# Kernel optimization log

Hardware: AMD Instinct MI355X
Metric: run time of the kernel (lower is better)

The kernel has to match this reference:

```python
import math
import jax, jax.numpy as jnp
import numpy as np

NUM_HEADS = 8
HEAD_DIM = 64
SCALE = 1.0 / math.sqrt(HEAD_DIM)


def setup_inputs() -> dict:
    key = jax.random.key(0)
    k1, k2, k3, k4 = jax.random.split(key, 4)
    B, C, H, W = 8, 256, 32, 32
    hidden = NUM_HEADS * HEAD_DIM  # 512
    x = jax.random.normal(k1, (B, C, H, W), dtype=jnp.float32)
    Wqkv = jax.random.normal(k2, (3 * hidden, C), dtype=jnp.float32) * 0.02  # 1x1 conv, no bias
    Wout = jax.random.normal(k3, (C, hidden), dtype=jnp.float32) * 0.02      # 1x1 conv weight
    bout = jax.random.normal(k4, (C,), dtype=jnp.float32) * 0.02             # 1x1 conv bias
    return {"x": x, "Wqkv": Wqkv, "Wout": Wout, "bout": bout}


def reference(x, Wqkv, Wout, bout):
    B, C, H, W = x.shape
    n = H * W
    # _AttLayer: 1x1 conv -> channels ordered (k=3, heads, head_dim)
    qkv = jnp.einsum('bcxy,oc->boxy', x, Wqkv)            # [B, 3*h*d, H, W]
    qkv = qkv.reshape(B, 3, NUM_HEADS, HEAD_DIM, n)       # 'b (k h d) x y -> b k h d (x y)'
    Q, K, V = qkv[:, 0], qkv[:, 1], qkv[:, 2]             # each [B, h, d, n]
    # CalcAtt: scaled QK^T, stable softmax over j, then Att @ V
    att = jnp.einsum('bhdi,bhdj->bhij', Q, K) * SCALE     # [B, h, n, n]
    att = jax.nn.softmax(att, axis=-1)                    # softmax already subtracts amax
    out = jnp.einsum('bhij,bhdj->bhid', att, V)           # [B, h, n, d]
    # 'b h (x y) d -> b (h d) x y'
    out = out.transpose(0, 1, 3, 2).reshape(B, NUM_HEADS * HEAD_DIM, H, W)
    # _AttOutLayer: 1x1 conv with bias
    return jnp.einsum('boxy,co->bcxy', out, Wout) + bout[None, :, None, None]
```

## Files before the change

kernel.cpp:

```cpp
#include <hip/hip_runtime.h>
#include <math.h>

#define NH 8
#define HD 64
#define NTOK 1024
#define CIN 256
#define HIDDEN 512
#define O3 1536
#define BATCH 8
#define ATT_SCALE 0.125f

typedef unsigned short u16;
typedef __attribute__((ext_vector_type(8))) short s16x8;
typedef __attribute__((ext_vector_type(4))) float f32x4;
typedef __attribute__((ext_vector_type(4))) unsigned short u16x4;

__device__ __forceinline__ u16 f2bf(float f) {
    union { float f; unsigned int u; } v; v.f = f;
    v.u += 0x7fff + ((v.u >> 16) & 1);
    return (u16)(v.u >> 16);
}
__device__ __forceinline__ float bf2f(u16 h) {
    union { unsigned int u; float f; } v; v.u = (unsigned)h << 16;
    return v.f;
}
__device__ __forceinline__ void split2(float x, u16& hi, u16& lo) {
    const u16 h = f2bf(x);
    hi = h;
    lo = f2bf(x - bf2f(h));
}

__device__ __forceinline__ s16x8 ldf(const u16* buf, int row, int chunk) {
    const int byte = (row * 128 + chunk * 16) ^ ((row & 7) << 4);
    return *(const s16x8*)((const char*)buf + byte);
}
__device__ __forceinline__ void st32(u16* buf, int row, int ch, s16x8 a, s16x8 b) {
    char* p = (char*)buf;
    *(s16x8*)(p + ((row * 128 + ch * 32) ^ ((row & 7) << 4)))      = a;
    *(s16x8*)(p + ((row * 128 + ch * 32 + 16) ^ ((row & 7) << 4))) = b;
}
__device__ __forceinline__ void st_stage(u16* buf, int t, s16x8 v0, s16x8 v1) {
    const int row = t >> 2, ch = t & 3;
    *(s16x8*)((char*)buf + ((row * 128 + ch * 16)       ^ ((row & 7) << 4))) = v0;
    *(s16x8*)((char*)buf + ((row * 128 + (ch + 4) * 16) ^ ((row & 7) << 4))) = v1;
}
__device__ __forceinline__ float hmax4(f32x4 v) {
    return fmaxf(fmaxf(v[0], v[1]), fmaxf(v[2], v[3]));
}
__device__ __forceinline__ float hsum4(f32x4 v) {
    return (v[0] + v[1]) + (v[2] + v[3]);
}

__global__ __launch_bounds__(256)
void split_f32(const float* __restrict__ src, u16* __restrict__ hi,
               u16* __restrict__ lo, int n4)
{
    const int i = blockIdx.x * 256 + threadIdx.x;
    if (i >= n4) return;
    const float4 v = ((const float4*)src)[i];
    u16 h0,h1,h2,h3,l0,l1,l2,l3;
    split2(v.x,h0,l0); split2(v.y,h1,l1); split2(v.z,h2,l2); split2(v.w,h3,l3);
    u16x4 H = {h0,h1,h2,h3}, L = {l0,l1,l2,l3};
    ((u16x4*)hi)[i] = H;
    ((u16x4*)lo)[i] = L;
}

__global__ __launch_bounds__(256)
void xpose_x(const float* __restrict__ x, u16* __restrict__ xthi,
             u16* __restrict__ xtlo)
{
    __shared__ float T[64][68];
    const int t  = threadIdx.x;
    const int p0 = blockIdx.x * 64;
    const int c0 = blockIdx.y * 64;
    const int b  = blockIdx.z;
    const int cl = t >> 4, pj = (t & 15) * 4;
    #pragma unroll
    for (int k = 0; k < 4; ++k)
        *(float4*)&T[cl + 16 * k][pj] =
            *(const float4*)&x[((size_t)b * CIN + c0 + cl + 16 * k) * NTOK + p0 + pj];
    __syncthreads();
    const int p = t >> 2, ch = t & 3;
    u16* dhi = xthi + ((size_t)b * NTOK + p0 + p) * CIN + c0 + ch * 16;
    u16* dlo = xtlo + ((size_t)b * NTOK + p0 + p) * CIN + c0 + ch * 16;
    #pragma unroll
    for (int g = 0; g < 2; ++g) {
        s16x8 H, L;
        #pragma unroll
        for (int e = 0; e < 8; ++e) {
            u16 hh, ll;
            split2(T[ch * 16 + g * 8 + e][p], hh, ll);
            H[e] = (short)hh; L[e] = (short)ll;
        }
        *(s16x8*)(dhi + g * 8) = H;
        *(s16x8*)(dlo + g * 8) = L;
    }
}

__global__ __launch_bounds__(256, 4)
void gemm_qkv_mfma(const u16* __restrict__ Whi, const u16* __restrict__ Wlo,
                   const u16* __restrict__ Xhi, const u16* __restrict__ Xlo,
                   u16* __restrict__ qkt, u16* __restrict__ vd)
{
    __shared__ __align__(16) char smem[32768];
    u16* Ah = (u16*)smem;
    u16* Al = (u16*)(smem + 8192);
    u16* Bh = (u16*)(smem + 16384);
    u16* Bl = (u16*)(smem + 24576);

    const int t = threadIdx.x;
    const int lane = t & 63, w = t >> 6;
    const int lr = lane & 15, lq = lane >> 4;
    const int p0 = blockIdx.x * 64;
    const int m0 = blockIdx.y * 64;
    const int b  = blockIdx.z;
    const int row = t >> 2, ch = t & 3;

    const u16* wh = Whi + (size_t)(m0 + row) * CIN + ch * 16;
    const u16* wl = Wlo + (size_t)(m0 + row) * CIN + ch * 16;
    const u16* xh = Xhi + ((size_t)b * NTOK + p0 + row) * CIN + ch * 16;
    const u16* xl = Xlo + ((size_t)b * NTOK + p0 + row) * CIN + ch * 16;

    f32x4 acc[4] = {};
    for (int kc = 0; kc < CIN; kc += 64) {
        __syncthreads();
        st32(Ah, row, ch, *(const s16x8*)(wh + kc), *(const s16x8*)(wh + kc + 8));
        st32(Al, row, ch, *(const s16x8*)(wl + kc), *(const s16x8*)(wl + kc + 8));
        st32(Bh, row, ch, *(const s16x8*)(xh + kc), *(const s16x8*)(xh + kc + 8));
        st32(Bl, row, ch, *(const s16x8*)(xl + kc), *(const s16x8*)(xl + kc + 8));
        __syncthreads();
        #pragma unroll
        for (int ks = 0; ks < 2; ++ks) {
            const s16x8 ah = ldf(Ah, w * 16 + lr, ks * 4 + lq);
            const s16x8 al = ldf(Al, w * 16 + lr, ks * 4 + lq);
            #pragma unroll
            for (int js = 0; js < 4; ++js) {
                const s16x8 bh = ldf(Bh, js * 16 + lr, ks * 4 + lq);
                const s16x8 bl = ldf(Bl, js * 16 + lr, ks * 4 + lq);
                acc[js] = __builtin_amdgcn_mfma_f32_16x16x32_bf16(ah, bh, acc[js], 0, 0, 0);
                acc[js] = __builtin_amdgcn_mfma_f32_16x16x32_bf16(al, bh, acc[js], 0, 0, 0);
                acc[js] = __builtin_amdgcn_mfma_f32_16x16x32_bf16(ah, bl, acc[js], 0, 0, 0);
            }
        }
    }

    __syncthreads();
    u16* T = Ah;
    char* Tc = (char*)T;
    if (m0 < 1024) {
        const float scale = (m0 < 512) ? ATT_SCALE : 1.0f;
        #pragma unroll
        for (int js = 0; js < 4; ++js) {
            const int p = js * 16 + lr;
            #pragma unroll
            for (int r = 0; r < 4; ++r) {
                const int o = w * 16 + lq * 4 + r;
                *(u16*)(Tc + ((p * 128 + o * 2) ^ ((p & 7) << 4))) = f2bf(acc[js][r] * scale);
            }
        }
        __syncthreads();
        const int sidx = (m0 < 512) ? 0 : 1;
        const int h = (m0 & 511) >> 6;
        u16* dst = qkt + ((((size_t)b * 2 + sidx) * NH + h) * NTOK + p0 + row) * 64 + ch * 16;
        *(s16x8*)dst       = *(const s16x8*)(Tc + ((row * 128 + ch * 32)      ^ ((row & 7) << 4)));
        *(s16x8*)(dst + 8) = *(const s16x8*)(Tc + ((row * 128 + ch * 32 + 16) ^ ((row & 7) << 4)));
    } else {
        const int h = (m0 - 1024) >> 6;
        #pragma unroll
        for (int js = 0; js < 4; ++js) {
            const int p = js * 16 + lr;
            #pragma unroll
            for (int r = 0; r < 4; ++r) {
                const int o = w * 16 + lq * 4 + r;
                *(u16*)(Tc + ((o * 128 + p * 2) ^ ((o & 7) << 4))) = f2bf(acc[js][r]);
            }
        }
        __syncthreads();
        u16* dst = vd + (((size_t)b * NH + h) * 64 + row) * NTOK + p0 + ch * 16;
        *(s16x8*)dst       = *(const s16x8*)(Tc + ((row * 128 + ch * 32)      ^ ((row & 7) << 4)));
        *(s16x8*)(dst + 8) = *(const s16x8*)(Tc + ((row * 128 + ch * 32 + 16) ^ ((row & 7) << 4)));
    }
}

__global__ __launch_bounds__(256, 4)
void attn_kernel(const u16* __restrict__ qkt, const u16* __restrict__ vd,
                 float* __restrict__ attn_out)
{
    __shared__ __align__(16) u16 Qt[64 * 64];
    __shared__ __align__(16) u16 Kt[64 * 64];
    __shared__ __align__(16) u16 Vt[64 * 64];
    __shared__ __align__(16) u16 Ps[64 * 64];

    const int t    = threadIdx.x;
    const int lane = t & 63;
    const int w    = t >> 6;
    const int lr   = lane & 15;
    const int lq   = lane >> 4;

    const int bid     = blockIdx.x;
    const int logical = (bid & 7) * 128 + (bid >> 3);
    const int it = logical & 15;
    const int h  = (logical >> 4) & 7;
    const int b  = logical >> 7;
    const int i0 = it * 64;

    const int srow = t >> 2, sch = t & 3;
    const u16* qg = qkt + ((((size_t)b * 2 + 0) * NH + h) * NTOK + i0 + srow) * 64 + sch * 8;
    const u16* kg = qkt + ((((size_t)b * 2 + 1) * NH + h) * NTOK + srow) * 64 + sch * 8;
    const u16* vg = vd  + (((size_t)b * NH + h) * 64 + srow) * NTOK + sch * 8;

    st_stage(Qt, t, *(const s16x8*)qg, *(const s16x8*)(qg + 32));

    s16x8 k0 = *(const s16x8*)kg, k1 = *(const s16x8*)(kg + 32);
    s16x8 v0 = *(const s16x8*)vg, v1 = *(const s16x8*)(vg + 32);

    f32x4 o0 = {0.f,0.f,0.f,0.f}, o1 = o0, o2 = o0, o3 = o0;
    float m_run = -INFINITY, l_run = 0.0f;

    const int ii = w * 16 + lr;
    char* pr = (char*)Ps;

    for (int jt = 0; jt < 16; ++jt) {
        __syncthreads();
        st_stage(Kt, t, k0, k1);
        st_stage(Vt, t, v0, v1);
        const int jn = (jt + 1) & 15;
        k0 = *(const s16x8*)(kg + (size_t)jn * 4096);
        k1 = *(const s16x8*)(kg + (size_t)jn * 4096 + 32);
        v0 = *(const s16x8*)(vg + (size_t)jn * 64);
        v1 = *(const s16x8*)(vg + (size_t)jn * 64 + 32);
        __syncthreads();

        f32x4 s0 = {0.f,0.f,0.f,0.f}, s1 = s0, s2 = s0, s3 = s0;
        #pragma unroll
        for (int ks = 0; ks < 2; ++ks) {
            const s16x8 qb = ldf(Qt, w * 16 + lr, ks * 4 + lq);
            s0 = __builtin_amdgcn_mfma_f32_16x16x32_bf16(ldf(Kt,      lr, ks*4+lq), qb, s0, 0,0,0);
            s1 = __builtin_amdgcn_mfma_f32_16x16x32_bf16(ldf(Kt, 16 + lr, ks*4+lq), qb, s1, 0,0,0);
            s2 = __builtin_amdgcn_mfma_f32_16x16x32_bf16(ldf(Kt, 32 + lr, ks*4+lq), qb, s2, 0,0,0);
            s3 = __builtin_amdgcn_mfma_f32_16x16x32_bf16(ldf(Kt, 48 + lr, ks*4+lq), qb, s3, 0,0,0);
        }

        float mt = fmaxf(fmaxf(hmax4(s0), hmax4(s1)), fmaxf(hmax4(s2), hmax4(s3)));
        mt = fmaxf(mt, __shfl_xor(mt, 16));
        mt = fmaxf(mt, __shfl_xor(mt, 32));
        const float mnew = fmaxf(m_run, mt);
        const float corr = __expf(m_run - mnew);
        f32x4 p0v, p1v, p2v, p3v;
        #pragma unroll
        for (int r = 0; r < 4; ++r) {
            p0v[r] = __expf(s0[r] - mnew);
            p1v[r] = __expf(s1[r] - mnew);
            p2v[r] = __expf(s2[r] - mnew);
            p3v[r] = __expf(s3[r] - mnew);
        }
        float lt = (hsum4(p0v) + hsum4(p1v)) + (hsum4(p2v) + hsum4(p3v));
        lt += __shfl_xor(lt, 16);
        lt += __shfl_xor(lt, 32);
        l_run = l_run * corr + lt;
        m_run = mnew;

        {
            u16x4 a = { f2bf(p0v[0]), f2bf(p0v[1]), f2bf(p0v[2]), f2bf(p0v[3]) };
            u16x4 bq= { f2bf(p1v[0]), f2bf(p1v[1]), f2bf(p1v[2]), f2bf(p1v[3]) };
            u16x4 c = { f2bf(p2v[0]), f2bf(p2v[1]), f2bf(p2v[2]), f2bf(p2v[3]) };
            u16x4 d = { f2bf(p3v[0]), f2bf(p3v[1]), f2bf(p3v[2]), f2bf(p3v[3]) };
            *(u16x4*)(pr + ((ii * 128 + ( 0 + lq * 4) * 2) ^ ((ii & 7) << 4))) = a;
            *(u16x4*)(pr + ((ii * 128 + (16 + lq * 4) * 2) ^ ((ii & 7) << 4))) = bq;
            *(u16x4*)(pr + ((ii * 128 + (32 + lq * 4) * 2) ^ ((ii & 7) << 4))) = c;
            *(u16x4*)(pr + ((ii * 128 + (48 + lq * 4) * 2) ^ ((ii & 7) << 4))) = d;
        }

        o0 *= corr; o1 *= corr; o2 *= corr; o3 *= corr;

        #pragma unroll
        for (int ks = 0; ks < 2; ++ks) {
            const s16x8 pb = ldf(Ps, w * 16 + lr, ks * 4 + lq);
            o0 = __builtin_amdgcn_mfma_f32_16x16x32_bf16(ldf(Vt,      lr, ks*4+lq), pb, o0, 0,0,0);
            o1 = __builtin_amdgcn_mfma_f32_16x16x32_bf16(ldf(Vt, 16 + lr, ks*4+lq), pb, o1, 0,0,0);
            o2 = __builtin_amdgcn_mfma_f32_16x16x32_bf16(ldf(Vt, 32 + lr, ks*4+lq), pb, o2, 0,0,0);
            o3 = __builtin_amdgcn_mfma_f32_16x16x32_bf16(ldf(Vt, 48 + lr, ks*4+lq), pb, o3, 0,0,0);
        }
    }

    const float inv = 1.0f / l_run;
    float* og = attn_out + (((size_t)b * NH + h) * 64) * NTOK + i0 + w * 16 + lr;
    #pragma unroll
    for (int r = 0; r < 4; ++r) {
        og[(size_t)( 0 + lq * 4 + r) * NTOK] = o0[r] * inv;
        og[(size_t)(16 + lq * 4 + r) * NTOK] = o1[r] * inv;
        og[(size_t)(32 + lq * 4 + r) * NTOK] = o2[r] * inv;
        og[(size_t)(48 + lq * 4 + r) * NTOK] = o3[r] * inv;
    }
}

__global__ __launch_bounds__(256, 4)
void gemm_out_mfma(const u16* __restrict__ Whi, const u16* __restrict__ Wlo,
                   const float* __restrict__ attn, const float* __restrict__ bias,
                   float* __restrict__ out)
{
    __shared__ __align__(16) char smem[24576];
    u16* Ah = (u16*)smem;
    u16* Al = (u16*)(smem + 8192);
    u16* Bt = (u16*)(smem + 16384);

    const int t = threadIdx.x;
    const int lane = t & 63, w = t >> 6;
    const int lr = lane & 15, lq = lane >> 4;
    const int p0 = blockIdx.x * 64;
    const int m0 = blockIdx.y * 64;
    const int b  = blockIdx.z;
    const int row = t >> 2, ch = t & 3;

    const u16* wh = Whi + (size_t)(m0 + row) * HIDDEN + ch * 16;
    const u16* wl = Wlo + (size_t)(m0 + row) * HIDDEN + ch * 16;
    const float* ab = attn + (size_t)b * HIDDEN * NTOK + p0;
    const int btok = t & 63;
    const int bog  = (t >> 6) * 16;

    f32x4 acc[4] = {};
    for (int kc = 0; kc < HIDDEN; kc += 64) {
        __syncthreads();
        st32(Ah, row, ch, *(const s16x8*)(wh + kc), *(const s16x8*)(wh + kc + 8));
        st32(Al, row, ch, *(const s16x8*)(wl + kc), *(const s16x8*)(wl + kc + 8));
        {
            s16x8 H0, H1;
            #pragma unroll
            for (int e = 0; e < 8; ++e)
                H0[e] = (short)f2bf(ab[(size_t)(kc + bog + e) * NTOK + btok]);
            #pragma unroll
            for (int e = 0; e < 8; ++e)
                H1[e] = (short)f2bf(ab[(size_t)(kc + bog + 8 + e) * NTOK + btok]);
            char* bp = (char*)Bt;
            *(s16x8*)(bp + ((btok * 128 + bog * 2)      ^ ((btok & 7) << 4))) = H0;
            *(s16x8*)(bp + ((btok * 128 + bog * 2 + 16) ^ ((btok & 7) << 4))) = H1;
        }
        __syncthreads();
        #pragma unroll
        for (int ks = 0; ks < 2; ++ks) {
            const s16x8 ah = ldf(Ah, w * 16 + lr, ks * 4 + lq);
            const s16x8 al = ldf(Al, w * 16 + lr, ks * 4 + lq);
            #pragma unroll
            for (int js = 0; js < 4; ++js) {
                const s16x8 bh = ldf(Bt, js * 16 + lr, ks * 4 + lq);
                acc[js] = __builtin_amdgcn_mfma_f32_16x16x32_bf16(ah, bh, acc[js], 0, 0, 0);
                acc[js] = __builtin_amdgcn_mfma_f32_16x16x32_bf16(al, bh, acc[js], 0, 0, 0);
            }
        }
    }

    __syncthreads();
    float* T = (float*)smem;
    #pragma unroll
    for (int js = 0; js < 4; ++js) {
        const int p = js * 16 + lr;
        #pragma unroll
        for (int r = 0; r < 4; ++r)
            T[(w * 16 + lq * 4 + r) * 68 + p] = acc[js][r];
    }
    __syncthreads();
    const float bv = bias[m0 + row];
    float* dst = out + ((size_t)b * CIN + m0 + row) * NTOK + p0;
    #pragma unroll
    for (int q = 0; q < 4; ++q) {
        float4 v = *(const float4*)&T[row * 68 + ch * 4 + q * 16];
        v.x += bv; v.y += bv; v.z += bv; v.w += bv;
        *(float4*)&dst[ch * 4 + q * 16] = v;
    }
}

extern "C" void kernel_launch(void* const* d_in, const int* in_sizes, int n_in,
                              void* d_out, int out_size, void* d_ws, size_t ws_size,
                              hipStream_t stream)
{
    const float* x    = (const float*)d_in[0];
    const float* Wqkv = (const float*)d_in[1];
    const float* Wout = (const float*)d_in[2];
    const float* bout = (const float*)d_in[3];
    float* out = (float*)d_out;

    char* ws = (char*)d_ws;
    u16* Wqhi = (u16*)ws;                         ws += (size_t)O3 * CIN * 2;
    u16* Wqlo = (u16*)ws;                         ws += (size_t)O3 * CIN * 2;
    u16* Wohi = (u16*)ws;                         ws += (size_t)CIN * HIDDEN * 2;
    u16* Wolo = (u16*)ws;                         ws += (size_t)CIN * HIDDEN * 2;
    u16* xThi = (u16*)ws;                         ws += (size_t)BATCH * NTOK * CIN * 2;
    u16* xTlo = (u16*)ws;                         ws += (size_t)BATCH * NTOK * CIN * 2;
    u16* qkt  = (u16*)ws;                         ws += (size_t)BATCH * 2 * NH * NTOK * HD * 2;
    u16* vd   = (u16*)ws;                         ws += (size_t)BATCH * NH * HD * NTOK * 2;
    float* attn = (float*)ws;                     ws += (size_t)BATCH * HIDDEN * NTOK * 4;

    split_f32<<<dim3(O3 * CIN / 1024), 256, 0, stream>>>(Wqkv, Wqhi, Wqlo, O3 * CIN / 4);
    split_f32<<<dim3(CIN * HIDDEN / 1024), 256, 0, stream>>>(Wout, Wohi, Wolo, CIN * HIDDEN / 4);
    xpose_x<<<dim3(16, 4, BATCH), 256, 0, stream>>>(x, xThi, xTlo);

    gemm_qkv_mfma<<<dim3(16, 24, BATCH), 256, 0, stream>>>(Wqhi, Wqlo, xThi, xTlo, qkt, vd);
    attn_kernel<<<dim3(1024), 256, 0, stream>>>(qkt, vd, attn);
    gemm_out_mfma<<<dim3(16, 4, BATCH), 256, 0, stream>>>(Wohi, Wolo, attn, bout, out);
}
```

Baseline: 144.6 us.

## Use exp2 softmax with lazy rescaling, hoist Q fragments, merge weight split kernels

Folds log2(e) into the Q scale so softmax can use exp2f. The running max is now updated only when a tile's max exceeds it by more than 8, which skips the correction multiply on most tiles. Q fragments are loaded from shared memory once before the key loop instead of every iteration, and the two weight-splitting launches are merged into one. The lazy rescale allows unnormalized probabilities up to 2^8, which adds a small bf16 precision risk in P.

```diff
diff --git a/kernel.cpp b/kernel.cpp
--- a/kernel.cpp
+++ b/kernel.cpp
@@ -9,6 +9,7 @@
 #define O3 1536
 #define BATCH 8
 #define ATT_SCALE 0.125f
+#define LOG2E 1.44269504f
 
 typedef unsigned short u16;
 typedef __attribute__((ext_vector_type(8))) short s16x8;
@@ -52,11 +53,19 @@
 }
 
 __global__ __launch_bounds__(256)
-void split_f32(const float* __restrict__ src, u16* __restrict__ hi,
-               u16* __restrict__ lo, int n4)
-{
-    const int i = blockIdx.x * 256 + threadIdx.x;
-    if (i >= n4) return;
+void split_both(const float* __restrict__ srcA, u16* __restrict__ hiA,
+                u16* __restrict__ loA, int n4A,
+                const float* __restrict__ srcB, u16* __restrict__ hiB,
+                u16* __restrict__ loB, int n4B)
+{
+    int i = blockIdx.x * 256 + threadIdx.x;
+    const float* src; u16 *hi, *lo;
+    if (i < n4A) { src = srcA; hi = hiA; lo = loA; }
+    else {
+        i -= n4A;
+        if (i >= n4B) return;
+        src = srcB; hi = hiB; lo = loB;
+    }
     const float4 v = ((const float4*)src)[i];
     u16 h0,h1,h2,h3,l0,l1,l2,l3;
     split2(v.x,h0,l0); split2(v.y,h1,l1); split2(v.z,h2,l2); split2(v.w,h3,l3);
@@ -148,7 +157,7 @@
     u16* T = Ah;
     char* Tc = (char*)T;
     if (m0 < 1024) {
-        const float scale = (m0 < 512) ? ATT_SCALE : 1.0f;
+        const float scale = (m0 < 512) ? ATT_SCALE * LOG2E : 1.0f;
         #pragma unroll
         for (int js = 0; js < 4; ++js) {
             const int p = js * 16 + lr;
@@ -214,6 +223,10 @@
     s16x8 k0 = *(const s16x8*)kg, k1 = *(const s16x8*)(kg + 32);
     s16x8 v0 = *(const s16x8*)vg, v1 = *(const s16x8*)(vg + 32);
 
+    __syncthreads();
+    const s16x8 qb0 = ldf(Qt, w * 16 + lr, lq);
+    const s16x8 qb1 = ldf(Qt, w * 16 + lr, 4 + lq);
+
     f32x4 o0 = {0.f,0.f,0.f,0.f}, o1 = o0, o2 = o0, o3 = o0;
     float m_run = -INFINITY, l_run = 0.0f;
 
@@ -232,33 +245,37 @@
         __syncthreads();
 
         f32x4 s0 = {0.f,0.f,0.f,0.f}, s1 = s0, s2 = s0, s3 = s0;
-        #pragma unroll
-        for (int ks = 0; ks < 2; ++ks) {
-            const s16x8 qb = ldf(Qt, w * 16 + lr, ks * 4 + lq);
-            s0 = __builtin_amdgcn_mfma_f32_16x16x32_bf16(ldf(Kt,      lr, ks*4+lq), qb, s0, 0,0,0);
-            s1 = __builtin_amdgcn_mfma_f32_16x16x32_bf16(ldf(Kt, 16 + lr, ks*4+lq), qb, s1, 0,0,0);
-            s2 = __builtin_amdgcn_mfma_f32_16x16x32_bf16(ldf(Kt, 32 + lr, ks*4+lq), qb, s2, 0,0,0);
-            s3 = __builtin_amdgcn_mfma_f32_16x16x32_bf16(ldf(Kt, 48 + lr, ks*4+lq), qb, s3, 0,0,0);
-        }
+        s0 = __builtin_amdgcn_mfma_f32_16x16x32_bf16(ldf(Kt,      lr, lq), qb0, s0, 0,0,0);
+        s1 = __builtin_amdgcn_mfma_f32_16x16x32_bf16(ldf(Kt, 16 + lr, lq), qb0, s1, 0,0,0);
+        s2 = __builtin_amdgcn_mfma_f32_16x16x32_bf16(ldf(Kt, 32 + lr, lq), qb0, s2, 0,0,0);
+        s3 = __builtin_amdgcn_mfma_f32_16x16x32_bf16(ldf(Kt, 48 + lr, lq), qb0, s3, 0,0,0);
+        s0 = __builtin_amdgcn_mfma_f32_16x16x32_bf16(ldf(Kt,      lr, 4 + lq), qb1, s0, 0,0,0);
+        s1 = __builtin_amdgcn_mfma_f32_16x16x32_bf16(ldf(Kt, 16 + lr, 4 + lq), qb1, s1, 0,0,0);
+        s2 = __builtin_amdgcn_mfma_f32_16x16x32_bf16(ldf(Kt, 32 + lr, 4 + lq), qb1, s2, 0,0,0);
+        s3 = __builtin_amdgcn_mfma_f32_16x16x32_bf16(ldf(Kt, 48 + lr, 4 + lq), qb1, s3, 0,0,0);
 
         float mt = fmaxf(fmaxf(hmax4(s0), hmax4(s1)), fmaxf(hmax4(s2), hmax4(s3)));
         mt = fmaxf(mt, __shfl_xor(mt, 16));
         mt = fmaxf(mt, __shfl_xor(mt, 32));
-        const float mnew = fmaxf(m_run, mt);
-        const float corr = __expf(m_run - mnew);
+        if (!__all(mt - m_run <= 8.0f)) {
+            const float mnew = fmaxf(m_run, mt);
+            const float corr = exp2f(m_run - mnew);
+            l_run *= corr;
+            o0 *= corr; o1 *= corr; o2 *= corr; o3 *= corr;
+            m_run = mnew;
+        }
         f32x4 p0v, p1v, p2v, p3v;
         #pragma unroll
         for (int r = 0; r < 4; ++r) {
-            p0v[r] = __expf(s0[r] - mnew);
-            p1v[r] = __expf(s1[r] - mnew);
-            p2v[r] = __expf(s2[r] - mnew);
-            p3v[r] = __expf(s3[r] - mnew);
+            p0v[r] = exp2f(s0[r] - m_run);
+            p1v[r] = exp2f(s1[r] - m_run);
+            p2v[r] = exp2f(s2[r] - m_run);
+            p3v[r] = exp2f(s3[r] - m_run);
         }
         float lt = (hsum4(p0v) + hsum4(p1v)) + (hsum4(p2v) + hsum4(p3v));
         lt += __shfl_xor(lt, 16);
         lt += __shfl_xor(lt, 32);
-        l_run = l_run * corr + lt;
-        m_run = mnew;
+        l_run += lt;
 
         {
             u16x4 a = { f2bf(p0v[0]), f2bf(p0v[1]), f2bf(p0v[2]), f2bf(p0v[3]) };
@@ -270,8 +287,6 @@
             *(u16x4*)(pr + ((ii * 128 + (32 + lq * 4) * 2) ^ ((ii & 7) << 4))) = c;
             *(u16x4*)(pr + ((ii * 128 + (48 + lq * 4) * 2) ^ ((ii & 7) << 4))) = d;
         }
-
-        o0 *= corr; o1 *= corr; o2 *= corr; o3 *= corr;
 
         #pragma unroll
         for (int ks = 0; ks < 2; ++ks) {
@@ -390,8 +405,9 @@
     u16* vd   = (u16*)ws;                         ws += (size_t)BATCH * NH * HD * NTOK * 2;
     float* attn = (float*)ws;                     ws += (size_t)BATCH * HIDDEN * NTOK * 4;
 
-    split_f32<<<dim3(O3 * CIN / 1024), 256, 0, stream>>>(Wqkv, Wqhi, Wqlo, O3 * CIN / 4);
-    split_f32<<<dim3(CIN * HIDDEN / 1024), 256, 0, stream>>>(Wout, Wohi, Wolo, CIN * HIDDEN / 4);
+    const int n4A = O3 * CIN / 4, n4B = CIN * HIDDEN / 4;
+    split_both<<<dim3((n4A + n4B + 255) / 256), 256, 0, stream>>>(
+        Wqkv, Wqhi, Wqlo, n4A, Wout, Wohi, Wolo, n4B);
     xpose_x<<<dim3(16, 4, BATCH), 256, 0, stream>>>(x, xThi, xTlo);
 
     gemm_qkv_mfma<<<dim3(16, 24, BATCH), 256, 0, stream>>>(Wqhi, Wqlo, xThi, xTlo, qkt, vd);
```

New measurement: 144.4 us. No clear change (-0.1%).
